# Optimization experiments

Hardware: AMD Instinct MI355X
Metric: run time of the kernel (lower is better)

The kernel has to match this reference:

```python
import jax, jax.numpy as jnp
import numpy as np

B = 8
C = 256
N40, N20, N10 = 1600, 400, 100
N = N40 + N20 + N10  # 2100 pixel nodes (40x40 + 20x20 + 10x10)

def _grid_edges(h, w, off):
    # 8-neighborhood 'contextual' edges within one scale's grid
    idx = np.arange(h * w).reshape(h, w)
    srcs, dsts = [], []
    for di in (-1, 0, 1):
        for dj in (-1, 0, 1):
            if di == 0 and dj == 0:
                continue
            s = idx[max(0, -di):h - max(0, di), max(0, -dj):w - max(0, dj)]
            d = idx[max(0, di):h - max(0, -di), max(0, dj):w - max(0, -dj)]
            srcs.append(off + s.ravel())
            dsts.append(off + d.ravel())
    return srcs, dsts

def _hier_edges(ph, pw, poff, coff):
    # bidirected parent <-> 4-children 'hierarchical' edges between scales
    i, j = np.meshgrid(np.arange(ph), np.arange(pw), indexing='ij')
    parent = (poff + i * pw + j).ravel()
    srcs, dsts = [], []
    cw = 2 * pw
    for di in (0, 1):
        for dj in (0, 1):
            child = (coff + (2 * i + di) * cw + (2 * j + dj)).ravel()
            srcs += [parent, child]
            dsts += [child, parent]
    return srcs, dsts

def build_edges():
    loop = [np.arange(N)]  # dgl.add_self_loop on both etypes
    cs, cd = [], []
    for (h, w, off) in ((40, 40, 0), (20, 20, N40), (10, 10, N40 + N20)):
        s, d = _grid_edges(h, w, off)
        cs += s; cd += d
    ctx_src = np.concatenate(cs + loop); ctx_dst = np.concatenate(cd + loop)
    hs, hd = [], []
    s, d = _hier_edges(20, 20, N40, 0); hs += s; hd += d
    s, d = _hier_edges(10, 10, N40 + N20, N40); hs += s; hd += d
    hier_src = np.concatenate(hs + loop); hier_dst = np.concatenate(hd + loop)
    return (jnp.asarray(ctx_src, jnp.int32), jnp.asarray(ctx_dst, jnp.int32),
            jnp.asarray(hier_src, jnp.int32), jnp.asarray(hier_dst, jnp.int32))

def _bn_relu(x, g, b, m, v):
    # inference-mode BatchNorm2d + ReLU
    scale = g * jax.lax.rsqrt(v + 1e-5)
    return jax.nn.relu(x * scale[:, None, None] + (b - m * scale)[:, None, None])

def _conv1x1(x, w, b):
    return jnp.einsum('bchw,oc->bohw', x, w) + b[:, None, None]

def _avgpool2(x):
    b, c, h, w = x.shape
    return x.reshape(b, c, h // 2, 2, w // 2, 2).mean(axis=(3, 5))

def _up2(x):
    return jnp.repeat(jnp.repeat(x, 2, axis=2), 2, axis=3)

def _gnn(h, src, dst, deg_inv, w, b):
    # gather -> scatter-add -> mean over in-neighbors (incl. self loop) -> linear -> ReLU
    agg = jnp.zeros_like(h).at[:, dst].add(h[:, src]) * deg_inv[None, :, None]
    return jax.nn.relu(jnp.einsum('bnc,cd->bnd', agg, w) + b)

def _convT2x2(x, wt, b):
    # stride-2 2x2 transposed conv; wt: [Cin, Cout, 2, 2] (torch layout)
    bsz, cin, h, w = x.shape
    y = jnp.einsum('bchw,cokl->bohkwl', x, wt)
    return y.reshape(bsz, wt.shape[1], 2 * h, 2 * w) + b[:, None, None]

def setup_inputs():
    key = jax.random.key(0)
    ks = iter(jax.random.split(key, 64))
    def rn(shape, scale=0.02):
        return jax.random.normal(next(ks), shape, jnp.float32) * scale
    inp = {}
    inp['feat0'] = rn((B, 256, 160, 160), 1.0)
    inp['feat1'] = rn((B, 512, 80, 80), 1.0)
    inp['feat2'] = rn((B, 1024, 40, 40), 1.0)
    inp['feat3'] = rn((B, 2048, 20, 20), 1.0)
    for i, cin in ((1, 512), (2, 1024), (3, 2048)):
        inp['dw%d' % i] = rn((256, cin))
        inp['db%d' % i] = jnp.zeros((256,), jnp.float32)
        inp['g%d' % i] = jnp.ones((256,), jnp.float32)
        inp['b%d' % i] = jnp.zeros((256,), jnp.float32)
        inp['m%d' % i] = jnp.zeros((256,), jnp.float32)
        inp['v%d' % i] = jnp.ones((256,), jnp.float32)
    for i in range(1, 7):
        inp['gW%d' % i] = rn((256, 256))
        inp['gb%d' % i] = jnp.zeros((256,), jnp.float32)
    for i, cout in ((1, 512), (2, 1024), (3, 2048)):
        inp['tW%d' % i] = rn((256, cout, 2, 2))
        inp['tb%d' % i] = jnp.zeros((cout,), jnp.float32)
    ctx_src, ctx_dst, hier_src, hier_dst = build_edges()
    inp['ctx_src'] = ctx_src; inp['ctx_dst'] = ctx_dst
    inp['hier_src'] = hier_src; inp['hier_dst'] = hier_dst
    return inp

def reference(feat0, feat1, feat2, feat3,
              dw1, db1, g1, b1, m1, v1,
              dw2, db2, g2, b2, m2, v2,
              dw3, db3, g3, b3, m3, v3,
              gW1, gb1, gW2, gb2, gW3, gb3, gW4, gb4, gW5, gb5, gW6, gb6,
              tW1, tb1, tW2, tb2, tW3, tb3,
              ctx_src, ctx_dst, hier_src, hier_dst):
    f40 = _avgpool2(_bn_relu(_conv1x1(feat1, dw1, db1), g1, b1, m1, v1))  # [B,256,40,40]
    f20 = _avgpool2(_bn_relu(_conv1x1(feat2, dw2, db2), g2, b2, m2, v2))  # [B,256,20,20]
    f10 = _avgpool2(_bn_relu(_conv1x1(feat3, dw3, db3), g3, b3, m3, v3))  # [B,256,10,10]
    bsz = f40.shape[0]
    # cnn_gnn: flatten all three scales into [B, 2100, 256] node features (batched
    # version of the original per-sample python loop; graph is identical per sample)
    h = jnp.concatenate([
        f40.reshape(bsz, C, N40).transpose(0, 2, 1),
        f20.reshape(bsz, C, N20).transpose(0, 2, 1),
        f10.reshape(bsz, C, N10).transpose(0, 2, 1)], axis=1)
    dic = 1.0 / jnp.zeros((N,), h.dtype).at[ctx_dst].add(1.0)
    dih = 1.0 / jnp.zeros((N,), h.dtype).at[hier_dst].add(1.0)
    # context1, context2, hierarch1, hierarch2, context4, context5
    h = _gnn(h, ctx_src, ctx_dst, dic, gW1, gb1)
    h = _gnn(h, ctx_src, ctx_dst, dic, gW2, gb2)
    h = _gnn(h, hier_src, hier_dst, dih, gW3, gb3)
    h = _gnn(h, hier_src, hier_dst, dih, gW4, gb4)
    h = _gnn(h, ctx_src, ctx_dst, dic, gW5, gb5)
    h = _gnn(h, ctx_src, ctx_dst, dic, gW6, gb6)
    # gnn_cnn: split back to NCHW maps
    f40g = h[:, :N40].transpose(0, 2, 1).reshape(bsz, C, 40, 40)
    f20g = h[:, N40:N40 + N20].transpose(0, 2, 1).reshape(bsz, C, 20, 20)
    f10g = h[:, N40 + N20:].transpose(0, 2, 1).reshape(bsz, C, 10, 10)
    f10_ref = f10 + f10g
    f20_ref = f20 + f20g + _up2(f10g)
    f40_ref = f40 + f40g + _up2(f20g)
    out1 = _convT2x2(f40_ref, tW1, tb1) + feat1
    out2 = _convT2x2(f20_ref, tW2, tb2) + feat2
    out3 = _convT2x2(f10_ref, tW3, tb3) + feat3
    return (feat0, out1, out2, out3)
```

## Files before the change

### kernel.cpp

```cpp
#include <hip/hip_runtime.h>
#include <cstdint>

#define NODES 2100

typedef __attribute__((ext_vector_type(8))) __bf16 bf16x8;
typedef __attribute__((ext_vector_type(4))) float f32x4;
typedef __attribute__((ext_vector_type(8))) unsigned short u16x8;

__device__ inline float bf2f(unsigned short s) { return __uint_as_float(((unsigned)s) << 16); }
__device__ inline unsigned short f2bf(float f) {
    unsigned u = __float_as_uint(f);
    u += 0x7fff + ((u >> 16) & 1);
    return (unsigned short)(u >> 16);
}

__device__ inline size_t pk(int row, int k, int nK) {
    return ((size_t)((row >> 4) * nK + (k >> 5)) << 9)
         + ((((k >> 3) & 3) << 4) + (row & 15)) * 8 + (k & 7);
}

struct PrepArgs {
    const float *dw0, *dw1, *dw2;
    const float *gw0, *gw1, *gw2, *gw3, *gw4, *gw5;
    const float *tw0, *tw1, *tw2;
    const float *g0, *g1, *g2, *b0, *b1, *b2, *m0, *m1, *m2, *v0, *v1, *v2, *db0, *db1, *db2;
    unsigned short *dwb, *gWTb, *tWTb;
    float *scshb;
};

__device__ inline void transpose32p(const float* __restrict__ in, unsigned short* __restrict__ outT,
                                    int Ccols, int c0, int r0)
{
    __shared__ float T[32][33];
    const int tx = threadIdx.x & 31, ty = threadIdx.x >> 5;
#pragma unroll
    for (int i = 0; i < 4; ++i)
        T[ty + i * 8][tx] = in[(size_t)(r0 + ty + i * 8) * Ccols + c0 + tx];
    __syncthreads();
#pragma unroll
    for (int i = 0; i < 4; ++i) {
        int Rrow = c0 + ty + i * 8;
        int k    = r0 + tx;
        outT[pk(Rrow, k, 8)] = f2bf(T[tx][ty + i * 8]);
    }
}

__global__ __launch_bounds__(256)
void mega_prep(PrepArgs a)
{
    int bid = blockIdx.x;
    const int t = threadIdx.x;
    if (bid < 448) {
        int idx = (bid * 256 + t) * 8;
        const float* src; unsigned short* dst; int loc, K;
        if (idx < 131072)      { src = a.dw0; dst = a.dwb;          loc = idx;          K = 512; }
        else if (idx < 393216) { src = a.dw1; dst = a.dwb + 131072; loc = idx - 131072; K = 1024; }
        else                   { src = a.dw2; dst = a.dwb + 393216; loc = idx - 393216; K = 2048; }
        int row = loc / K, k = loc - row * K;
        float4 x = *(const float4*)(src + loc);
        float4 y = *(const float4*)(src + loc + 4);
        u16x8 r;
        r[0] = f2bf(x.x); r[1] = f2bf(x.y); r[2] = f2bf(x.z); r[3] = f2bf(x.w);
        r[4] = f2bf(y.x); r[5] = f2bf(y.y); r[6] = f2bf(y.z); r[7] = f2bf(y.w);
        *(u16x8*)(dst + pk(row, k, K >> 5)) = r;
    } else if (bid < 832) {
        int gid = bid - 448;
        int l = gid >> 6, sb = gid & 63;
        const float* gw[6] = {a.gw0, a.gw1, a.gw2, a.gw3, a.gw4, a.gw5};
        transpose32p(gw[l], a.gWTb + (size_t)l * 65536, 256, (sb & 7) << 5, (sb >> 3) << 5);
    } else if (bid < 4416) {
        int gid = bid - 832;
        const float* tw; unsigned short* dst; int ncx, loc;
        if (gid < 512)       { tw = a.tw0; dst = a.tWTb;           ncx = 64;  loc = gid; }
        else if (gid < 1536) { tw = a.tw1; dst = a.tWTb + 524288;  ncx = 128; loc = gid - 512; }
        else                 { tw = a.tw2; dst = a.tWTb + 1572864; ncx = 256; loc = gid - 1536; }
        int cx = loc % ncx, ry = loc / ncx;
        transpose32p(tw, dst, ncx * 32, cx << 5, ry << 5);
    } else {
        const float* g[3]  = {a.g0, a.g1, a.g2};
        const float* b[3]  = {a.b0, a.b1, a.b2};
        const float* m[3]  = {a.m0, a.m1, a.m2};
        const float* v[3]  = {a.v0, a.v1, a.v2};
        const float* db[3] = {a.db0, a.db1, a.db2};
        for (int s = 0; s < 3; ++s) {
            float sc = g[s][t] * rsqrtf(v[s][t] + 1e-5f);
            a.scshb[s * 512 + t] = sc;
            a.scshb[s * 512 + 256 + t] = (db[s][t] - m[s][t]) * sc + b[s][t];
        }
    }
}

struct ConvArgs {
    const float* feat[3];
    const unsigned short* dwb[3];
    const float* scsh[3];
    unsigned short* h0out;
};

__global__ __launch_bounds__(256)
void conv_fused(ConvArgs ca)
{
    __shared__ __align__(16) unsigned short As[2][64 * 64];
    int bx = blockIdx.x;
    int s, mt;
    if (bx < 800)       { s = 0; mt = bx; }
    else if (bx < 1000) { s = 1; mt = bx - 800; }
    else                { s = 2; mt = bx - 1000; }
    const int Kc[3]  = {512, 1024, 2048};
    const int Wc[3]  = {80, 40, 20};
    const int PPc[3] = {1600, 400, 100};
    const int nfc[3] = {0, 1600, 2000};
    const int K = Kc[s], W = Wc[s], W2 = W >> 1, HW = W * W, PP = PPc[s], noff = nfc[s];
    const int nK = K >> 5;
    const float* feat = ca.feat[s];
    const unsigned short* dw = ca.dwb[s];
    const float* scsh = ca.scsh[s];

    const int t = threadIdx.x, lane = t & 63, w = t >> 6;
    const int sx = (lane & 7) << 4;

    const int ml = t & 63;
    const int kw = t >> 6;
    const int graw = mt * 64 + ml;
    const int b = graw / HW;
    const int rem = graw - b * HW;
    const int pooled = rem >> 2, sub = rem & 3;
    const int pi = pooled / W2, pj = pooled - pi * W2;
    const int i = pi * 2 + (sub >> 1), j = pj * 2 + (sub & 1);
    const float* src = feat + (size_t)b * K * HW + (size_t)i * W + j;
    const int sxm = (ml & 7) << 3;

    f32x4 acc[4][4];
#pragma unroll
    for (int fr = 0; fr < 4; ++fr)
#pragma unroll
        for (int fc = 0; fc < 4; ++fc) acc[fr][fc] = (f32x4){0.f, 0.f, 0.f, 0.f};

    int buf = 0;
    for (int k0 = 0; k0 < K; k0 += 64) {
        float v[16];
#pragma unroll
        for (int it = 0; it < 16; ++it)
            v[it] = src[(size_t)(k0 + it * 4 + kw) * HW];
        unsigned short* Ab = As[buf];
#pragma unroll
        for (int it = 0; it < 16; ++it) {
            int k_l = it * 4 + kw;
            Ab[(ml << 6) + (k_l ^ sxm)] = f2bf(v[it]);
        }
        __syncthreads();
#pragma unroll
        for (int kk = 0; kk < 2; ++kk) {
            bf16x8 a[4], bb[4];
#pragma unroll
            for (int f = 0; f < 4; ++f) {
                int pa = ((((f * 16 + (lane & 15)) << 7) + kk * 64 + ((lane >> 4) << 4)) ^ sx);
                a[f] = *(const bf16x8*)((const char*)Ab + pa);
                bb[f] = *(const bf16x8*)(dw + ((size_t)(((w << 2) + f) * nK + (k0 >> 5) + kk) << 9) + (lane << 3));
            }
#pragma unroll
            for (int fr = 0; fr < 4; ++fr)
#pragma unroll
                for (int fc = 0; fc < 4; ++fc)
                    acc[fr][fc] = __builtin_amdgcn_mfma_f32_16x16x32_bf16(a[fr], bb[fc], acc[fr][fc], 0, 0, 0);
        }
        buf ^= 1;
    }

#pragma unroll
    for (int fc = 0; fc < 4; ++fc) {
        const int o = w * 64 + fc * 16 + (lane & 15);
        const float sc = scsh[o], sh = scsh[256 + o];
#pragma unroll
        for (int fr = 0; fr < 4; ++fr) {
            const int mrow = mt * 64 + fr * 16 + (lane >> 4) * 4;
            const int q = mrow >> 2;
            const int bi = q / PP;
            const int node = noff + (q - bi * PP);
            float sum = 0.f;
#pragma unroll
            for (int r = 0; r < 4; ++r)
                sum += fmaxf(acc[fr][fc][r] * sc + sh, 0.f);
            ca.h0out[((size_t)(bi * NODES + node)) * 256 + o] = f2bf(sum * 0.25f);
        }
    }
}

__global__ __launch_bounds__(256)
void gnn_fused(const unsigned short* __restrict__ h, const unsigned short* __restrict__ BT,
               const float* __restrict__ bias, unsigned short* __restrict__ out, int hier)
{
    __shared__ __align__(16) unsigned short As[2][32 * 64];
    const int t = threadIdx.x, lane = t & 63, w = t >> 6;
    const int r0 = blockIdx.x << 5;
    const int myrow = t >> 3, q = t & 7;
    const int grow = r0 + myrow;
    const int b = grow / NODES;
    const int n = grow - b * NODES;

    int gw, off;
    if (n < 1600)      { gw = 40; off = 0; }
    else if (n < 2000) { gw = 20; off = 1600; }
    else               { gw = 10; off = 2000; }
    const int li = (n - off) / gw;
    const int lj = (n - off) - li * gw;
    int nbr[9]; int cnt = 0;
    if (!hier) {
#pragma unroll
        for (int di = -1; di <= 1; ++di)
#pragma unroll
            for (int dj = -1; dj <= 1; ++dj) {
                int ii = li + di, jj = lj + dj;
                if (ii >= 0 && ii < gw && jj >= 0 && jj < gw) nbr[cnt++] = off + ii * gw + jj;
            }
    } else {
        nbr[cnt++] = n;
        if (off == 0) {
            nbr[cnt++] = 1600 + (li >> 1) * 20 + (lj >> 1);
        } else if (off == 1600) {
            nbr[cnt++] = 2000 + (li >> 1) * 10 + (lj >> 1);
#pragma unroll
            for (int di = 0; di < 2; ++di)
#pragma unroll
                for (int dj = 0; dj < 2; ++dj)
                    nbr[cnt++] = ((li << 1) + di) * 40 + ((lj << 1) + dj);
        } else {
#pragma unroll
            for (int di = 0; di < 2; ++di)
#pragma unroll
                for (int dj = 0; dj < 2; ++dj)
                    nbr[cnt++] = 1600 + ((li << 1) + di) * 20 + ((lj << 1) + dj);
        }
    }
    int nboff[9];
#pragma unroll
    for (int e = 0; e < 9; ++e)
        nboff[e] = (b * NODES + nbr[e < cnt ? e : 0]) * 256 + q * 8;
    const float inv = 1.0f / (float)cnt;
    const int sx = (lane & 7) << 4;
    const int awr = (myrow << 6) + ((q ^ (myrow & 7)) << 3);

    f32x4 acc[2][4];
#pragma unroll
    for (int fr = 0; fr < 2; ++fr)
#pragma unroll
        for (int fc = 0; fc < 4; ++fc) acc[fr][fc] = (f32x4){0.f, 0.f, 0.f, 0.f};

    u16x8 pre[9];
#pragma unroll
    for (int e = 0; e < 9; ++e) pre[e] = *(const u16x8*)(h + nboff[e]);

    int buf = 0;
    for (int k0 = 0; k0 < 256; k0 += 64) {
        float sacc[8] = {0, 0, 0, 0, 0, 0, 0, 0};
#pragma unroll
        for (int e = 0; e < 9; ++e) {
            if (e < cnt) {
#pragma unroll
                for (int jj = 0; jj < 8; ++jj) sacc[jj] += bf2f(pre[e][jj]);
            }
        }
        u16x8 o0;
#pragma unroll
        for (int jj = 0; jj < 8; ++jj) o0[jj] = f2bf(sacc[jj] * inv);
        *(u16x8*)&As[buf][awr] = o0;
        __syncthreads();

        const int k0n = (k0 + 64) & 255;
#pragma unroll
        for (int e = 0; e < 9; ++e) pre[e] = *(const u16x8*)(h + nboff[e] + k0n);

        const unsigned short* Ab = As[buf];
#pragma unroll
        for (int kk = 0; kk < 2; ++kk) {
            bf16x8 a[2], bb[4];
#pragma unroll
            for (int f = 0; f < 2; ++f) {
                int pa = ((((f * 16 + (lane & 15)) << 7) + kk * 64 + ((lane >> 4) << 4)) ^ sx);
                a[f] = *(const bf16x8*)((const char*)Ab + pa);
            }
#pragma unroll
            for (int f = 0; f < 4; ++f)
                bb[f] = *(const bf16x8*)(BT + ((size_t)(((w << 2) + f) * 8 + (k0 >> 5) + kk) << 9) + (lane << 3));
#pragma unroll
            for (int fr = 0; fr < 2; ++fr)
#pragma unroll
                for (int fc = 0; fc < 4; ++fc)
                    acc[fr][fc] = __builtin_amdgcn_mfma_f32_16x16x32_bf16(a[fr], bb[fc], acc[fr][fc], 0, 0, 0);
        }
        buf ^= 1;
    }

#pragma unroll
    for (int fc = 0; fc < 4; ++fc) {
        const int d = w * 64 + fc * 16 + (lane & 15);
        const float bv = bias[d];
#pragma unroll
        for (int fr = 0; fr < 2; ++fr) {
            int rb = r0 + fr * 16 + (lane >> 4) * 4;
#pragma unroll
            for (int r = 0; r < 4; ++r)
                out[(size_t)(rb + r) * 256 + d] = f2bf(fmaxf(acc[fr][fc][r] + bv, 0.f));
        }
    }
}

__global__ __launch_bounds__(256)
void a_build(const unsigned short* __restrict__ h0, const unsigned short* __restrict__ h6,
             unsigned short* __restrict__ Ao)
{
    int bx = blockIdx.x;
    int P, H2, noff, pbase, pw, haspar, rows; size_t aoff;
    if (bx < 1600)      { P = 1600; H2 = 40; noff = 0;    pbase = 1600; pw = 20; haspar = 1; aoff = 0;               rows = 12800; }
    else if (bx < 2000) { P = 400;  H2 = 20; noff = 1600; pbase = 2000; pw = 10; haspar = 1; aoff = 12800ULL * 256; rows = 3200; bx -= 1600; }
    else                { P = 100;  H2 = 10; noff = 2000; pbase = 0;    pw = 0;  haspar = 0; aoff = 16000ULL * 256; rows = 800;  bx -= 2000; }
    const int gid = bx * 256 + threadIdx.x;
    const int m = gid >> 5, c0 = (gid & 31) << 3;
    unsigned short* dst = Ao + aoff + (((size_t)((m >> 4) * 8 + (c0 >> 5))) << 9)
                        + ((((c0 >> 3) & 3) << 4) + (m & 15)) * 8;
    if (m >= rows) {
        u16x8 z = (u16x8){0, 0, 0, 0, 0, 0, 0, 0};
        *(u16x8*)dst = z;
        return;
    }
    const int b = m / P, pix = m - b * P;
    const size_t src = ((size_t)(b * NODES + noff + pix)) * 256 + c0;
    u16x8 x0 = *(const u16x8*)(h0 + src);
    u16x8 x6 = *(const u16x8*)(h6 + src);
    float v[8];
#pragma unroll
    for (int e = 0; e < 8; ++e) v[e] = bf2f(x0[e]) + bf2f(x6[e]);
    if (haspar) {
        int ii = pix / H2, jj = pix - ii * H2;
        size_t sp = ((size_t)(b * NODES + pbase + (ii >> 1) * pw + (jj >> 1))) * 256 + c0;
        u16x8 xp = *(const u16x8*)(h6 + sp);
#pragma unroll
        for (int e = 0; e < 8; ++e) v[e] += bf2f(xp[e]);
    }
    u16x8 r;
#pragma unroll
    for (int e = 0; e < 8; ++e) r[e] = f2bf(v[e]);
    *(u16x8*)dst = r;
}

struct ConvtArgs {
    const unsigned short* WT[3];
    const unsigned short* Apix[3];
    const float* tb[3];
    const float* feat[3];
    float* out[3];
    const float4* cps; float4* cpd;
};

__global__ __launch_bounds__(256)
void convt_fused(ConvtArgs ct)
{
    int bx = blockIdx.x;
    if (bx < 1024) {
        const int base = bx * 256 + threadIdx.x;
        const int stride = 1024 * 256;
        const float4* s = ct.cps;
        float4* d = ct.cpd;
        for (int j = 0; j < 50; j += 5) {
            float4 v0 = s[base + (size_t)(j + 0) * stride];
            float4 v1 = s[base + (size_t)(j + 1) * stride];
            float4 v2 = s[base + (size_t)(j + 2) * stride];
            float4 v3 = s[base + (size_t)(j + 3) * stride];
            float4 v4 = s[base + (size_t)(j + 4) * stride];
            d[base + (size_t)(j + 0) * stride] = v0;
            d[base + (size_t)(j + 1) * stride] = v1;
            d[base + (size_t)(j + 2) * stride] = v2;
            d[base + (size_t)(j + 3) * stride] = v3;
            d[base + (size_t)(j + 4) * stride] = v4;
        }
        return;
    }
    bx -= 1024;
    int s, px, my;
    if (bx < 6400) {
        s = 0;
        int L = (bx & 7) * 800 + (bx >> 3);
        px = L >> 5; my = L & 31;
    } else if (bx < 9600) {
        s = 1; bx -= 6400;
        int L = (bx & 7) * 400 + (bx >> 3);
        px = L >> 6; my = L & 63;
    } else {
        s = 2; bx -= 9600;
        int L = (bx & 7) * 208 + (bx >> 3);
        my = L / 13; px = L - my * 13;
    }
    const int Pc[3]  = {1600, 400, 100};
    const int H2c[3] = {40, 20, 10};
    const int Cc[3]  = {512, 1024, 2048};
    const int Mc[3]  = {12800, 3200, 800};
    const int P = Pc[s], H2 = H2c[s], Cout = Cc[s], Mpix = Mc[s];
    const int m0 = my << 6, n0 = px << 6;
    const unsigned short* WT = ct.WT[s];
    const unsigned short* Apix = ct.Apix[s];

    const int t = threadIdx.x, lane = t & 63, w = t >> 6;
    const int wr = w >> 1, wc = w & 1;

    size_t abase[2], bbase[2];
#pragma unroll
    for (int f = 0; f < 2; ++f) {
        abase[f] = ((size_t)(((m0 >> 4) + wr * 2 + f) * 8) << 9) + (lane << 3);
        bbase[f] = ((size_t)(((n0 >> 4) + wc * 2 + f) * 8) << 9) + (lane << 3);
    }

    f32x4 acc[2][2];
#pragma unroll
    for (int fr = 0; fr < 2; ++fr)
#pragma unroll
        for (int fc = 0; fc < 2; ++fc) acc[fr][fc] = (f32x4){0.f, 0.f, 0.f, 0.f};

    bf16x8 aC[2], bC[2], aN[2], bN[2];
#pragma unroll
    for (int f = 0; f < 2; ++f) {
        aC[f] = *(const bf16x8*)(WT   + abase[f]);
        bC[f] = *(const bf16x8*)(Apix + bbase[f]);
    }
#pragma unroll
    for (int c = 0; c < 8; ++c) {
        if (c < 7) {
#pragma unroll
            for (int f = 0; f < 2; ++f) {
                aN[f] = *(const bf16x8*)(WT   + abase[f] + ((size_t)(c + 1) << 9));
                bN[f] = *(const bf16x8*)(Apix + bbase[f] + ((size_t)(c + 1) << 9));
            }
        }
#pragma unroll
        for (int fr = 0; fr < 2; ++fr)
#pragma unroll
            for (int fc = 0; fc < 2; ++fc)
                acc[fr][fc] = __builtin_amdgcn_mfma_f32_16x16x32_bf16(aC[fr], bC[fc], acc[fr][fc], 0, 0, 0);
#pragma unroll
        for (int f = 0; f < 2; ++f) { aC[f] = aN[f]; bC[f] = bN[f]; }
    }

    const int H = H2 * 2;
    const float* feat = ct.feat[s];
    float* out = ct.out[s];
#pragma unroll
    for (int fc = 0; fc < 2; ++fc) {
        const int p_g = n0 + wc * 32 + fc * 16 + (lane & 15);
        if (p_g < Mpix) {
            const int b = p_g / P, pix = p_g - b * P;
            const int ii = pix / H2, jj = pix - ii * H2;
#pragma unroll
            for (int fr = 0; fr < 2; ++fr) {
                const int rb = m0 + wr * 32 + fr * 16 + (lane >> 4) * 4;
                const int o = rb >> 2;
                const float tbo = ct.tb[s][o];
                size_t base = (((size_t)(b * Cout + o)) * H + 2 * ii) * H + 2 * jj;
                float2 f0 = *(const float2*)&feat[base];
                float2 r0v; r0v.x = acc[fr][fc][0] + tbo + f0.x; r0v.y = acc[fr][fc][1] + tbo + f0.y;
                *(float2*)&out[base] = r0v;
                float2 f1 = *(const float2*)&feat[base + H];
                float2 r1v; r1v.x = acc[fr][fc][2] + tbo + f1.x; r1v.y = acc[fr][fc][3] + tbo + f1.y;
                *(float2*)&out[base + H] = r1v;
            }
        }
    }
}

extern "C" void kernel_launch(void* const* d_in, const int* in_sizes, int n_in,
                              void* d_out, int out_size, void* d_ws, size_t ws_size,
                              hipStream_t stream)
{
    const float* feats[3] = { (const float*)d_in[1], (const float*)d_in[2], (const float*)d_in[3] };
    const float* gb[6];
    for (int l = 0; l < 6; ++l) gb[l] = (const float*)d_in[23 + 2 * l];
    const float* tb[3] = { (const float*)d_in[35], (const float*)d_in[37], (const float*)d_in[39] };

    size_t off = 0;
    auto alloc = [&](size_t bytes) { size_t r = off; off = (off + bytes + 511) & ~(size_t)511; return r; };
    unsigned short* h0b  = (unsigned short*)((char*)d_ws + alloc(16800ULL * 256 * 2));
    unsigned short* hA   = (unsigned short*)((char*)d_ws + alloc(16800ULL * 256 * 2));
    unsigned short* hB   = (unsigned short*)((char*)d_ws + alloc(16800ULL * 256 * 2));
    unsigned short* dwb  = (unsigned short*)((char*)d_ws + alloc(917504ULL * 2));
    unsigned short* gWTb = (unsigned short*)((char*)d_ws + alloc(6ULL * 65536 * 2));
    unsigned short* tWTb = (unsigned short*)((char*)d_ws + alloc(3670016ULL * 2));
    float*          scshb= (float*)((char*)d_ws + alloc(3ULL * 512 * 4));
    unsigned short* Aconvt = (unsigned short*)((char*)d_ws + off);

    PrepArgs pa;
    pa.dw0 = (const float*)d_in[4];  pa.dw1 = (const float*)d_in[10]; pa.dw2 = (const float*)d_in[16];
    pa.gw0 = (const float*)d_in[22]; pa.gw1 = (const float*)d_in[24]; pa.gw2 = (const float*)d_in[26];
    pa.gw3 = (const float*)d_in[28]; pa.gw4 = (const float*)d_in[30]; pa.gw5 = (const float*)d_in[32];
    pa.tw0 = (const float*)d_in[34]; pa.tw1 = (const float*)d_in[36]; pa.tw2 = (const float*)d_in[38];
    pa.g0 = (const float*)d_in[6];  pa.g1 = (const float*)d_in[12]; pa.g2 = (const float*)d_in[18];
    pa.b0 = (const float*)d_in[7];  pa.b1 = (const float*)d_in[13]; pa.b2 = (const float*)d_in[19];
    pa.m0 = (const float*)d_in[8];  pa.m1 = (const float*)d_in[14]; pa.m2 = (const float*)d_in[20];
    pa.v0 = (const float*)d_in[9];  pa.v1 = (const float*)d_in[15]; pa.v2 = (const float*)d_in[21];
    pa.db0 = (const float*)d_in[5]; pa.db1 = (const float*)d_in[11]; pa.db2 = (const float*)d_in[17];
    pa.dwb = dwb; pa.gWTb = gWTb; pa.tWTb = tWTb; pa.scshb = scshb;
    mega_prep<<<dim3(4417), dim3(256), 0, stream>>>(pa);

    ConvArgs ca;
    ca.feat[0] = feats[0]; ca.feat[1] = feats[1]; ca.feat[2] = feats[2];
    ca.dwb[0] = dwb; ca.dwb[1] = dwb + 131072; ca.dwb[2] = dwb + 393216;
    ca.scsh[0] = scshb; ca.scsh[1] = scshb + 512; ca.scsh[2] = scshb + 1024;
    ca.h0out = h0b;
    conv_fused<<<dim3(1050), dim3(256), 0, stream>>>(ca);

    const int types[6] = {0, 0, 1, 1, 0, 0};
    const unsigned short* hin = h0b;
    unsigned short* houts[6] = {hA, hB, hA, hB, hA, hB};
    for (int l = 0; l < 6; ++l) {
        gnn_fused<<<dim3(525), dim3(256), 0, stream>>>(
            hin, gWTb + (size_t)l * 65536, gb[l], houts[l], types[l]);
        hin = houts[l];
    }
    unsigned short* h6 = hB;

    a_build<<<dim3(2104), dim3(256), 0, stream>>>(h0b, h6, Aconvt);

    ConvtArgs ct;
    ct.WT[0] = tWTb; ct.WT[1] = tWTb + 524288; ct.WT[2] = tWTb + 1572864;
    ct.Apix[0] = Aconvt; ct.Apix[1] = Aconvt + 12800ULL * 256; ct.Apix[2] = Aconvt + 16000ULL * 256;
    ct.tb[0] = tb[0]; ct.tb[1] = tb[1]; ct.tb[2] = tb[2];
    ct.feat[0] = feats[0]; ct.feat[1] = feats[1]; ct.feat[2] = feats[2];
    ct.out[0] = (float*)d_out + 52428800;
    ct.out[1] = (float*)d_out + 52428800 + 26214400;
    ct.out[2] = (float*)d_out + 52428800 + 26214400 + 13107200;
    ct.cps = (const float4*)d_in[0];
    ct.cpd = (float4*)d_out;
    convt_fused<<<dim3(1024 + 11264), dim3(256), 0, stream>>>(ct);
}
```

Before: 484.7 us.

## Prefetch next K-slab in pooled GEMM and stage convT tiles via LDS

In the pooled 1x1-conv GEMM, the next 64-wide K slab of fp32 activations is now loaded into registers while the current slab's MFMAs run, hiding global load latency. In the fused transposed-conv kernel, the A and B tiles are now brought into a double-buffered shared-memory area with direct global-to-LDS loads (global_load_lds). Each wave reads its fragments from LDS, so operand tiles are fetched once per block instead of redundantly by each wave. The cost is higher register pressure from the extra 16-float prefetch buffer and added block-wide barriers and LDS usage in the convT kernel, which may reduce occupancy.

```diff
diff --git a/kernel.cpp b/kernel.cpp
--- a/kernel.cpp
+++ b/kernel.cpp
@@ -12,6 +12,11 @@
     unsigned u = __float_as_uint(f);
     u += 0x7fff + ((u >> 16) & 1);
     return (unsigned short)(u >> 16);
+}
+__device__ inline void gload16(const unsigned short* g, void* lds) {
+    __builtin_amdgcn_global_load_lds(
+        (const __attribute__((address_space(1))) void*)g,
+        (__attribute__((address_space(3))) void*)lds, 16, 0, 0);
 }
 
 __device__ inline size_t pk(int row, int k, int nK) {
@@ -136,19 +141,25 @@
 #pragma unroll
         for (int fc = 0; fc < 4; ++fc) acc[fr][fc] = (f32x4){0.f, 0.f, 0.f, 0.f};
 
+    float vC[16], vN[16];
+#pragma unroll
+    for (int it = 0; it < 16; ++it)
+        vC[it] = src[(size_t)(it * 4 + kw) * HW];
+
     int buf = 0;
     for (int k0 = 0; k0 < K; k0 += 64) {
-        float v[16];
-#pragma unroll
-        for (int it = 0; it < 16; ++it)
-            v[it] = src[(size_t)(k0 + it * 4 + kw) * HW];
         unsigned short* Ab = As[buf];
 #pragma unroll
         for (int it = 0; it < 16; ++it) {
             int k_l = it * 4 + kw;
-            Ab[(ml << 6) + (k_l ^ sxm)] = f2bf(v[it]);
+            Ab[(ml << 6) + (k_l ^ sxm)] = f2bf(vC[it]);
         }
         __syncthreads();
+        if (k0 + 64 < K) {
+#pragma unroll
+            for (int it = 0; it < 16; ++it)
+                vN[it] = src[(size_t)(k0 + 64 + it * 4 + kw) * HW];
+        }
 #pragma unroll
         for (int kk = 0; kk < 2; ++kk) {
             bf16x8 a[4], bb[4];
@@ -164,6 +175,8 @@
                 for (int fc = 0; fc < 4; ++fc)
                     acc[fr][fc] = __builtin_amdgcn_mfma_f32_16x16x32_bf16(a[fr], bb[fc], acc[fr][fc], 0, 0, 0);
         }
+#pragma unroll
+        for (int it = 0; it < 16; ++it) vC[it] = vN[it];
         buf ^= 1;
     }
 
@@ -355,6 +368,7 @@
 __global__ __launch_bounds__(256)
 void convt_fused(ConvtArgs ct)
 {
+    __shared__ __align__(16) unsigned short Sb[2][16 * 512];
     int bx = blockIdx.x;
     if (bx < 1024) {
         const int base = bx * 256 + threadIdx.x;
@@ -396,18 +410,29 @@
     const int Mc[3]  = {12800, 3200, 800};
     const int P = Pc[s], H2 = H2c[s], Cout = Cc[s], Mpix = Mc[s];
     const int m0 = my << 6, n0 = px << 6;
+    const int m0u = my << 2, n0u = px << 2;
     const unsigned short* WT = ct.WT[s];
     const unsigned short* Apix = ct.Apix[s];
 
     const int t = threadIdx.x, lane = t & 63, w = t >> 6;
     const int wr = w >> 1, wc = w & 1;
 
-    size_t abase[2], bbase[2];
-#pragma unroll
-    for (int f = 0; f < 2; ++f) {
-        abase[f] = ((size_t)(((m0 >> 4) + wr * 2 + f) * 8) << 9) + (lane << 3);
-        bbase[f] = ((size_t)(((n0 >> 4) + wc * 2 + f) * 8) << 9) + (lane << 3);
-    }
+    auto STAGE = [&](int c, int bsel) {
+#pragma unroll
+        for (int ul = 0; ul < 4; ++ul) {
+            int u = (w << 2) + ul;
+            const unsigned short* src;
+            if (w < 2) {
+                int ru = u >> 1, ch = u & 1;
+                src = WT + ((size_t)((m0u + ru) * 8 + c * 2 + ch) << 9) + (lane << 3);
+            } else {
+                int v = u - 8;
+                int ru = v >> 1, ch = v & 1;
+                src = Apix + ((size_t)((n0u + ru) * 8 + c * 2 + ch) << 9) + (lane << 3);
+            }
+            gload16(src, (char*)&Sb[bsel][0] + u * 1024 + lane * 16);
+        }
+    };
 
     f32x4 acc[2][2];
 #pragma unroll
@@ -415,28 +440,27 @@
 #pragma unroll
         for (int fc = 0; fc < 2; ++fc) acc[fr][fc] = (f32x4){0.f, 0.f, 0.f, 0.f};
 
-    bf16x8 aC[2], bC[2], aN[2], bN[2];
-#pragma unroll
-    for (int f = 0; f < 2; ++f) {
-        aC[f] = *(const bf16x8*)(WT   + abase[f]);
-        bC[f] = *(const bf16x8*)(Apix + bbase[f]);
-    }
-#pragma unroll
-    for (int c = 0; c < 8; ++c) {
-        if (c < 7) {
+    STAGE(0, 0);
+    __syncthreads();
+#pragma unroll
+    for (int c = 0; c < 4; ++c) {
+        if (c < 3) STAGE(c + 1, (c + 1) & 1);
+        const unsigned short* B = &Sb[c & 1][0];
+#pragma unroll
+        for (int kk = 0; kk < 2; ++kk) {
+            bf16x8 a[2], bb[2];
 #pragma unroll
             for (int f = 0; f < 2; ++f) {
-                aN[f] = *(const bf16x8*)(WT   + abase[f] + ((size_t)(c + 1) << 9));
-                bN[f] = *(const bf16x8*)(Apix + bbase[f] + ((size_t)(c + 1) << 9));
-            }
-        }
-#pragma unroll
-        for (int fr = 0; fr < 2; ++fr)
-#pragma unroll
-            for (int fc = 0; fc < 2; ++fc)
-                acc[fr][fc] = __builtin_amdgcn_mfma_f32_16x16x32_bf16(aC[fr], bC[fc], acc[fr][fc], 0, 0, 0);
-#pragma unroll
-        for (int f = 0; f < 2; ++f) { aC[f] = aN[f]; bC[f] = bN[f]; }
+                a[f]  = *(const bf16x8*)(B + (((wr * 2 + f) * 2 + kk) << 9) + (lane << 3));
+                bb[f] = *(const bf16x8*)(B + ((8 + (wc * 2 + f) * 2 + kk) << 9) + (lane << 3));
+            }
+#pragma unroll
+            for (int fr = 0; fr < 2; ++fr)
+#pragma unroll
+                for (int fc = 0; fc < 2; ++fc)
+                    acc[fr][fc] = __builtin_amdgcn_mfma_f32_16x16x32_bf16(a[fr], bb[fc], acc[fr][fc], 0, 0, 0);
+        }
+        __syncthreads();
     }
 
     const int H = H2 * 2;
```

New measurement: 456.2 us. 5.9% less time.
